# Performance work log

Measured on AMD Instinct MI355X. Metric: run time of the kernel, lower is better.

The kernel has to match this reference:

```python
import jax, jax.numpy as jnp
import numpy as np

B, T_IN, T_OUT, ADIM, PDIM, EDIM = 32, 512, 2048, 384, 4, 1


def setup_inputs() -> dict:
    key = jax.random.key(0)
    ks = jax.random.split(key, 8)
    hs = jax.random.normal(ks[0], (B, T_IN, ADIM), dtype=jnp.float32)
    # durations in [1, 5) so max expanded length 4*T_IN == T_OUT (no truncation)
    durations = jax.random.randint(ks[1], (B, T_IN), 1, 5).astype(jnp.int64)
    input_lengths = (T_IN // 2 + jax.random.randint(ks[2], (B,), 0, T_IN // 2)).astype(jnp.int64)
    pitch_target = jax.random.normal(ks[3], (B, T_OUT, PDIM), dtype=jnp.float32)
    energy_target = jax.random.normal(ks[4], (B, T_OUT, EDIM), dtype=jnp.float32)
    duration_mask = jnp.zeros((B, T_IN, 1), dtype=bool)
    variance_mask = jnp.zeros((B, T_OUT, 1), dtype=bool)
    # kernel-size-1 ConvNorm weights (kernel dim squeezed) + biases
    pitch_w = jax.random.normal(ks[5], (ADIM, PDIM), dtype=jnp.float32) / np.sqrt(PDIM)
    pitch_b = jnp.zeros((ADIM,), dtype=jnp.float32)
    energy_w = jax.random.normal(ks[6], (ADIM, EDIM), dtype=jnp.float32) / np.sqrt(EDIM)
    energy_b = jnp.zeros((ADIM,), dtype=jnp.float32)
    return dict(hs=hs, durations=durations, input_lengths=input_lengths,
                pitch_target=pitch_target, energy_target=energy_target,
                duration_mask=duration_mask, variance_mask=variance_mask,
                pitch_w=pitch_w, pitch_b=pitch_b, energy_w=energy_w, energy_b=energy_b)


def length_regulate(xs, durations, input_lengths, t_out):
    # xs: [B, T_in, D]; durations: [B, T_in]; output: [B, t_out, D], zero-padded
    Bsz, Tin, D = xs.shape
    pos = jnp.arange(Tin)
    valid = pos[None, :] < input_lengths[:, None]            # [B, T_in]
    d = jnp.where(valid, durations, 0)
    total = d.sum(axis=-1)
    # torch: if d.sum()==0, fill truncated d with ones
    d = jnp.where((total == 0)[:, None] & valid, 1, d)
    cum = jnp.cumsum(d, axis=-1)                             # [B, T_in]
    t = jnp.arange(t_out)
    # source phone index per output frame: count of cum entries <= t
    idx = jax.vmap(lambda c: jnp.searchsorted(c, t, side='right'))(cum)  # [B, t_out]
    idx = jnp.clip(idx, 0, Tin - 1)
    out = jnp.take_along_axis(xs, idx[..., None], axis=1)    # [B, t_out, D]
    frame_mask = t[None, :] < cum[:, -1:]                    # [B, t_out]
    return jnp.where(frame_mask[..., None], out, jnp.zeros((), xs.dtype))


def reference(hs, durations, input_lengths, pitch_target, energy_target,
              duration_mask, variance_mask, pitch_w, pitch_b, energy_w, energy_b):
    hs = length_regulate(hs, durations, input_lengths, T_OUT)      # [B, T_out, adim]
    # kernel-size-1 convs == pointwise linear over channel dim (dropout rate 0)
    pitch_embed = jnp.einsum('btp,ap->bta', pitch_target, pitch_w) + pitch_b
    energy_embed = jnp.einsum('bte,ae->bta', energy_target, energy_w) + energy_b
    return hs + pitch_embed + energy_embed
```

## Files before the change

### kernel.cpp

```cpp
#include <hip/hip_runtime.h>

constexpr int kB    = 32;
constexpr int kTin  = 512;
constexpr int kTout = 2048;
constexpr int kA    = 384;
constexpr int kC4   = kA / 4;

__global__ __launch_bounds__(kTin) void lr_index_kernel(
    const int* __restrict__ durations,
    const int* __restrict__ input_lengths,
    int* __restrict__ idx_out)
{
    __shared__ int cum[kTin];
    const int b = blockIdx.x;
    const int t = threadIdx.x;
    const int len = input_lengths[b];
    const bool valid = t < len;
    int dval = valid ? durations[b * kTin + t] : 0;
    int total = 0;
    for (int pass = 0; pass < 2; ++pass) {
        __syncthreads();
        cum[t] = dval;
        __syncthreads();
        for (int off = 1; off < kTin; off <<= 1) {
            int add = (t >= off) ? cum[t - off] : 0;
            __syncthreads();
            cum[t] += add;
            __syncthreads();
        }
        total = cum[kTin - 1];
        if (total != 0) break;
        dval = valid ? 1 : 0;
    }
    for (int k = 0; k < kTout / kTin; ++k) {
        const int to = t + k * kTin;
        int lo = 0, hi = kTin;
        while (lo < hi) {
            const int mid = (lo + hi) >> 1;
            if (cum[mid] <= to) lo = mid + 1; else hi = mid;
        }
        int idx = (lo < kTin) ? lo : (kTin - 1);
        idx_out[b * kTout + to] = (to < total) ? idx : -1;
    }
}

__global__ __launch_bounds__(384) void fuse_kernel(
    const float*  __restrict__ hs,
    const int*    __restrict__ idx,
    const float4* __restrict__ pitch_t,
    const float*  __restrict__ energy_t,
    const float4* __restrict__ pitch_w,
    const float*  __restrict__ pitch_b,
    const float*  __restrict__ energy_w,
    const float*  __restrict__ energy_b,
    float4*       __restrict__ out)
{
    const int tid = threadIdx.x;
    const int c4  = tid % kC4;
    const int sub = tid / kC4;
    const int a0  = c4 * 4;

    const float4 w0 = pitch_w[a0];
    const float4 w1 = pitch_w[a0 + 1];
    const float4 w2 = pitch_w[a0 + 2];
    const float4 w3 = pitch_w[a0 + 3];
    const float4 ew = make_float4(energy_w[a0], energy_w[a0 + 1],
                                  energy_w[a0 + 2], energy_w[a0 + 3]);
    const float4 bias = make_float4(pitch_b[a0]     + energy_b[a0],
                                    pitch_b[a0 + 1] + energy_b[a0 + 1],
                                    pitch_b[a0 + 2] + energy_b[a0 + 2],
                                    pitch_b[a0 + 3] + energy_b[a0 + 3]);

    const long nrows = (long)kB * kTout;
    for (long row = (long)blockIdx.x * 4 + sub; row < nrows;
         row += 4L * gridDim.x) {
        const int src = idx[row];
        float4 h = make_float4(0.f, 0.f, 0.f, 0.f);
        if (src >= 0) {
            const long b = row >> 11;
            h = *(const float4*)(hs + (b * kTin + src) * (long)kA + a0);
        }
        const float4 pt = pitch_t[row];
        const float  e  = energy_t[row];
        float4 o;
        o.x = h.x + pt.x * w0.x + pt.y * w0.y + pt.z * w0.z + pt.w * w0.w + e * ew.x + bias.x;
        o.y = h.y + pt.x * w1.x + pt.y * w1.y + pt.z * w1.z + pt.w * w1.w + e * ew.y + bias.y;
        o.z = h.z + pt.x * w2.x + pt.y * w2.y + pt.z * w2.z + pt.w * w2.w + e * ew.z + bias.z;
        o.w = h.w + pt.x * w3.x + pt.y * w3.y + pt.z * w3.z + pt.w * w3.w + e * ew.w + bias.w;
        out[row * kC4 + c4] = o;
    }
}

extern "C" void kernel_launch(void* const* d_in, const int* in_sizes, int n_in,
                              void* d_out, int out_size, void* d_ws, size_t ws_size,
                              hipStream_t stream) {
    const float* hs            = (const float*)d_in[0];
    const int*   durations     = (const int*)d_in[1];
    const int*   input_lengths = (const int*)d_in[2];
    const float* pitch_t       = (const float*)d_in[3];
    const float* energy_t      = (const float*)d_in[4];
    const float* pitch_w       = (const float*)d_in[7];
    const float* pitch_b       = (const float*)d_in[8];
    const float* energy_w      = (const float*)d_in[9];
    const float* energy_b      = (const float*)d_in[10];
    float* out = (float*)d_out;
    int*   idx = (int*)d_ws;

    lr_index_kernel<<<kB, kTin, 0, stream>>>(durations, input_lengths, idx);
    fuse_kernel<<<1024, 384, 0, stream>>>(hs, idx,
        (const float4*)pitch_t, energy_t,
        (const float4*)pitch_w, pitch_b, energy_w, energy_b,
        (float4*)out);
}
```

Measured before the change: 156.6 us.

## Fuse length-regulator index computation into the output kernel with wave-level scan

Merges the separate index-building kernel into the main fused kernel. Each block recomputes the per-batch duration prefix sum using wavefront shuffle scans, then binary-searches source indices for its 64 output rows into shared memory. This removes one kernel launch and the global round trip for the index array, and output writes become nontemporal stores. The cost is redundant prefix-sum work, 32 blocks per batch each redoing it, plus a block-wide sync before the streaming phase.

```diff
diff --git a/kernel.cpp b/kernel.cpp
--- a/kernel.cpp
+++ b/kernel.cpp
@@ -5,89 +5,108 @@
 constexpr int kTout = 2048;
 constexpr int kA    = 384;
 constexpr int kC4   = kA / 4;
+constexpr int kBPB  = 32;
+constexpr int kRPB  = kTout / kBPB;
+constexpr int kSegs = kTin / 64;
 
-__global__ __launch_bounds__(kTin) void lr_index_kernel(
-    const int* __restrict__ durations,
-    const int* __restrict__ input_lengths,
-    int* __restrict__ idx_out)
+typedef float vf4 __attribute__((ext_vector_type(4)));
+
+__global__ __launch_bounds__(384) void fused_va_kernel(
+    const float* __restrict__ hs,
+    const int*   __restrict__ durations,
+    const int*   __restrict__ input_lengths,
+    const vf4*   __restrict__ pitch_t,
+    const float* __restrict__ energy_t,
+    const vf4*   __restrict__ pitch_w,
+    const float* __restrict__ pitch_b,
+    const float* __restrict__ energy_w,
+    const float* __restrict__ energy_b,
+    float*       __restrict__ out)
 {
     __shared__ int cum[kTin];
-    const int b = blockIdx.x;
-    const int t = threadIdx.x;
-    const int len = input_lengths[b];
-    const bool valid = t < len;
-    int dval = valid ? durations[b * kTin + t] : 0;
-    int total = 0;
-    for (int pass = 0; pass < 2; ++pass) {
-        __syncthreads();
-        cum[t] = dval;
-        __syncthreads();
-        for (int off = 1; off < kTin; off <<= 1) {
-            int add = (t >= off) ? cum[t - off] : 0;
-            __syncthreads();
-            cum[t] += add;
-            __syncthreads();
+    __shared__ int ssum[kSegs];
+    __shared__ int soff[kSegs + 1];
+    __shared__ int ridx[kRPB];
+
+    const int tid  = threadIdx.x;
+    const int b    = blockIdx.x / kBPB;
+    const int slot = blockIdx.x % kBPB;
+    const int row0 = slot * kRPB;
+
+    const int len  = input_lengths[b];
+    const int wave = tid >> 6;
+    const int lane = tid & 63;
+
+    for (int seg = wave; seg < kSegs; seg += 384 / 64) {
+        const int i = (seg << 6) + lane;
+        int dv = (i < len) ? durations[b * kTin + i] : 0;
+        #pragma unroll
+        for (int off = 1; off < 64; off <<= 1) {
+            const int n = __shfl_up(dv, off, 64);
+            if (lane >= off) dv += n;
         }
-        total = cum[kTin - 1];
-        if (total != 0) break;
-        dval = valid ? 1 : 0;
+        cum[i] = dv;
+        if (lane == 63) ssum[seg] = dv;
     }
-    for (int k = 0; k < kTout / kTin; ++k) {
-        const int to = t + k * kTin;
-        int lo = 0, hi = kTin;
-        while (lo < hi) {
-            const int mid = (lo + hi) >> 1;
-            if (cum[mid] <= to) lo = mid + 1; else hi = mid;
+    __syncthreads();
+    if (tid == 0) {
+        int s = 0;
+        #pragma unroll
+        for (int k = 0; k < kSegs; ++k) { soff[k] = s; s += ssum[k]; }
+        soff[kSegs] = s;
+    }
+    __syncthreads();
+    const int total = soff[kSegs];
+
+    if (tid < kRPB) {
+        const int to = row0 + tid;
+        int r = -1;
+        if (total == 0) {
+            if (to < len) r = to;
+        } else if (to < total) {
+            int lo = 0, hi = kTin;
+            while (lo < hi) {
+                const int mid = (lo + hi) >> 1;
+                if (cum[mid] + soff[mid >> 6] <= to) lo = mid + 1; else hi = mid;
+            }
+            r = (lo < kTin) ? lo : (kTin - 1);
         }
-        int idx = (lo < kTin) ? lo : (kTin - 1);
-        idx_out[b * kTout + to] = (to < total) ? idx : -1;
+        ridx[tid] = r;
     }
-}
+    __syncthreads();
 
-__global__ __launch_bounds__(384) void fuse_kernel(
-    const float*  __restrict__ hs,
-    const int*    __restrict__ idx,
-    const float4* __restrict__ pitch_t,
-    const float*  __restrict__ energy_t,
-    const float4* __restrict__ pitch_w,
-    const float*  __restrict__ pitch_b,
-    const float*  __restrict__ energy_w,
-    const float*  __restrict__ energy_b,
-    float4*       __restrict__ out)
-{
-    const int tid = threadIdx.x;
-    const int c4  = tid % kC4;
+    const int c4 = tid % kC4;
     const int sub = tid / kC4;
-    const int a0  = c4 * 4;
+    const int a0 = c4 * 4;
 
-    const float4 w0 = pitch_w[a0];
-    const float4 w1 = pitch_w[a0 + 1];
-    const float4 w2 = pitch_w[a0 + 2];
-    const float4 w3 = pitch_w[a0 + 3];
-    const float4 ew = make_float4(energy_w[a0], energy_w[a0 + 1],
-                                  energy_w[a0 + 2], energy_w[a0 + 3]);
-    const float4 bias = make_float4(pitch_b[a0]     + energy_b[a0],
-                                    pitch_b[a0 + 1] + energy_b[a0 + 1],
-                                    pitch_b[a0 + 2] + energy_b[a0 + 2],
-                                    pitch_b[a0 + 3] + energy_b[a0 + 3]);
+    const vf4 w0 = pitch_w[a0];
+    const vf4 w1 = pitch_w[a0 + 1];
+    const vf4 w2 = pitch_w[a0 + 2];
+    const vf4 w3 = pitch_w[a0 + 3];
+    const vf4 ew = { energy_w[a0], energy_w[a0 + 1],
+                     energy_w[a0 + 2], energy_w[a0 + 3] };
+    const vf4 bias = { pitch_b[a0]     + energy_b[a0],
+                       pitch_b[a0 + 1] + energy_b[a0 + 1],
+                       pitch_b[a0 + 2] + energy_b[a0 + 2],
+                       pitch_b[a0 + 3] + energy_b[a0 + 3] };
 
-    const long nrows = (long)kB * kTout;
-    for (long row = (long)blockIdx.x * 4 + sub; row < nrows;
-         row += 4L * gridDim.x) {
-        const int src = idx[row];
-        float4 h = make_float4(0.f, 0.f, 0.f, 0.f);
-        if (src >= 0) {
-            const long b = row >> 11;
-            h = *(const float4*)(hs + (b * kTin + src) * (long)kA + a0);
-        }
-        const float4 pt = pitch_t[row];
-        const float  e  = energy_t[row];
-        float4 o;
+    const long rowbase = (long)b * kTout + row0;
+    #pragma unroll 4
+    for (int it = 0; it < kRPB / 4; ++it) {
+        const int  rl  = (it << 2) + sub;
+        const long row = rowbase + rl;
+        const int  src = ridx[rl];
+        vf4 h = { 0.f, 0.f, 0.f, 0.f };
+        if (src >= 0)
+            h = *(const vf4*)(hs + ((long)b * kTin + src) * kA + a0);
+        const vf4   pt = pitch_t[row];
+        const float e  = energy_t[row];
+        vf4 o;
         o.x = h.x + pt.x * w0.x + pt.y * w0.y + pt.z * w0.z + pt.w * w0.w + e * ew.x + bias.x;
         o.y = h.y + pt.x * w1.x + pt.y * w1.y + pt.z * w1.z + pt.w * w1.w + e * ew.y + bias.y;
         o.z = h.z + pt.x * w2.x + pt.y * w2.y + pt.z * w2.z + pt.w * w2.w + e * ew.z + bias.z;
         o.w = h.w + pt.x * w3.x + pt.y * w3.y + pt.z * w3.z + pt.w * w3.w + e * ew.w + bias.w;
-        out[row * kC4 + c4] = o;
+        __builtin_nontemporal_store(o, (vf4*)(out + row * kA + a0));
     }
 }
 
@@ -104,11 +123,10 @@
     const float* energy_w      = (const float*)d_in[9];
     const float* energy_b      = (const float*)d_in[10];
     float* out = (float*)d_out;
-    int*   idx = (int*)d_ws;
 
-    lr_index_kernel<<<kB, kTin, 0, stream>>>(durations, input_lengths, idx);
-    fuse_kernel<<<1024, 384, 0, stream>>>(hs, idx,
-        (const float4*)pitch_t, energy_t,
-        (const float4*)pitch_w, pitch_b, energy_w, energy_b,
-        (float4*)out);
+    fused_va_kernel<<<kB * kBPB, 384, 0, stream>>>(
+        hs, durations, input_lengths,
+        (const vf4*)pitch_t, energy_t,
+        (const vf4*)pitch_w, pitch_b, energy_w, energy_b,
+        out);
 }
```

Result: no change. 155.3 us (-0.9%).
